# Optimization experiments

Hardware: AMD Instinct MI355X
Metric: run time of the kernel (lower is better)

The kernel has to match this reference:

```python
import jax, jax.numpy as jnp
import numpy as np

N = 20000      # nodes (human PPI network scale)
E = 640000     # edges (avg degree 32)
PE, GOS, PROT = 128, 128, 480
OM_DIMS = [3, 3, 24, 24]          # transcriptome, proteome, effectome, interactome
D = 384                           # latent_space_dimension = 128 * 3 (jk 'cat')
H = 128                           # hidden_channels per layer
NEG_SLOPE = 0.1


def setup_inputs() -> dict:
    key = jax.random.key(0)
    ks = jax.random.split(key, 64)
    rn = lambda k, shp, s=0.05: jax.random.normal(k, shp, jnp.float32) * s
    inp = {
        "x": jax.random.normal(ks[0], (N, PE + GOS + PROT), jnp.float32),
        "x_ft": jax.random.normal(ks[1], (N, sum(OM_DIMS)), jnp.float32),
        "edge_index": jax.random.randint(ks[2], (2, E), 0, N),
    }
    i = 3
    def lin(fin, fout, name):
        nonlocal i
        inp["W_" + name] = rn(ks[i], (fin, fout)); inp["b_" + name] = jnp.zeros((fout,), jnp.float32)
        i += 1
    lin(PE, D, "pe"); lin(GOS, D, "gos"); lin(PROT, D, "prot")
    for j, d in enumerate(OM_DIMS):
        lin(d, D, f"om{j}")
    dims = [D, H, H, H]
    for j in range(3):
        lin(dims[j], dims[j + 1], f"c{j}")   # feature-branch GCN convs
        lin(dims[j], dims[j + 1], f"o{j}")   # omics-branch GCN convs
    lin(2 * D, D, "lat")
    lin(D, H, "drug"); lin(D, H, "dis")
    lin(H, 2, "odrug"); lin(H, 2, "odis")
    return inp


def _gcn(x, W, b, src, dst, deg_inv):
    # GCNConv(improved=True): A_hat = A + 2I, sym norm D^-1/2 A_hat D^-1/2
    h = x @ W                                  # [N, F_out]
    coef = deg_inv[src] * deg_inv[dst]         # [E]
    agg = jax.ops.segment_sum(h[src] * coef[:, None], dst, num_segments=N)
    agg = agg + h * (2.0 * deg_inv * deg_inv)[:, None]   # self loops (weight 2)
    return agg + b


def reference(x, x_ft, edge_index,
              W_pe, b_pe, W_gos, b_gos, W_prot, b_prot,
              W_om0, b_om0, W_om1, b_om1, W_om2, b_om2, W_om3, b_om3,
              W_c0, b_c0, W_o0, b_o0, W_c1, b_c1, W_o1, b_o1, W_c2, b_c2, W_o2, b_o2,
              W_lat, b_lat, W_drug, b_drug, W_dis, b_dis,
              W_odrug, b_odrug, W_odis, b_odis):
    act = lambda t: jax.nn.leaky_relu(t, NEG_SLOPE)
    src, dst = edge_index[0], edge_index[1]
    deg = jax.ops.segment_sum(jnp.ones((E,), jnp.float32), dst, num_segments=N) + 2.0
    deg_inv = jax.lax.rsqrt(deg)

    # encoders (features branch): pe | gosemsim | prot_emb slices of x
    pe = x[:, :PE]; gos = x[:, PE:PE + GOS]; prot = x[:, PE + GOS:PE + GOS + PROT]
    h = act(pe @ W_pe + b_pe + gos @ W_gos + b_gos + prot @ W_prot + b_prot)

    # encoders (omics branch): 3|3|24|24 slices of x_ft
    offs = np.cumsum([0] + OM_DIMS)
    Wom = [W_om0, W_om1, W_om2, W_om3]; bom = [b_om0, b_om1, b_om2, b_om3]
    g = act(sum(x_ft[:, offs[j]:offs[j + 1]] @ Wom[j] + bom[j] for j in range(4)))

    Wc = [W_c0, W_c1, W_c2]; bc = [b_c0, b_c1, b_c2]
    Wo = [W_o0, W_o1, W_o2]; bo = [b_o0, b_o1, b_o2]
    hs, gs = [], []
    for j in range(3):
        h = act(_gcn(h, Wc[j], bc[j], src, dst, deg_inv)); hs.append(h)
        g = act(_gcn(g, Wo[j], bo[j], src, dst, deg_inv)); gs.append(g)
    jk = jnp.concatenate(hs, axis=-1)          # [N, 384]
    jk_om = jnp.concatenate(gs, axis=-1)       # [N, 384]

    z = act(jnp.concatenate([jk, jk_om], axis=-1) @ W_lat + b_lat)  # [N, 384]
    drug = act(z @ W_drug + b_drug) @ W_odrug + b_odrug             # [N, 2]
    dis = act(z @ W_dis + b_dis) @ W_odis + b_odis                  # [N, 2]
    return jnp.concatenate([drug, dis], axis=-1)                    # [N, 4]
```

## Files before the change

kernel.cpp:

```cpp
#include <hip/hip_runtime.h>
#include <cstdint>

#define NN 20000
#define NNP 20096
#define NE 640000
#define NEG_SLOPE 0.1f
#define NP4 4
#define PSZ 5000
#define CAP 48

typedef unsigned short ushort_t;
typedef __attribute__((ext_vector_type(8))) short short8;
typedef __attribute__((ext_vector_type(4))) float f32x4;

__device__ __forceinline__ unsigned short f2bf(float f) {
    union { float f; unsigned u; } v; v.f = f;
    unsigned r = v.u + 0x7fffu + ((v.u >> 16) & 1u);
    return (unsigned short)(r >> 16);
}
__device__ __forceinline__ float bflo(unsigned u) { return __uint_as_float(u << 16); }
__device__ __forceinline__ float bfhi(unsigned u) { return __uint_as_float(u & 0xffff0000u); }

__device__ __forceinline__ int swz(int r) { return (r ^ (r >> 2)) & 3; }

__device__ __forceinline__ void gld_lds16(const void* g, void* l) {
    __builtin_amdgcn_global_load_lds(
        (const __attribute__((address_space(1))) void*)g,
        (__attribute__((address_space(3))) void*)l,
        16, 0, 0);
}

#define O_CAT   0
#define O_OM    282624
#define O_C0    307200
#define O_O0    356352
#define O_C1    405504
#define O_O1    421888
#define O_C2    438272
#define O_O2    454656
#define O_LAT   471040
#define O_HEADS 765952
#define WT_TOTAL 864256

#define PACK_TOTAL (WT_TOTAL + 384 + 384 + 256)
#define CVT_T1 (NN * 736 / 4)
#define P1_FILLB (NE / 256)
#define P1_CVTB ((CVT_T1 + NN * 64 + 255) / 256)
#define P1_PKB  (PACK_TOTAL / 256)

__global__ __launch_bounds__(256) void phase1(
    const int* __restrict__ esrc, const int* __restrict__ edst,
    int* __restrict__ cnt4, unsigned* __restrict__ bkt,
    const float* __restrict__ x, const float* __restrict__ xft,
    ushort_t* __restrict__ xb, ushort_t* __restrict__ xftb,
    const float* __restrict__ Wpe, const float* __restrict__ Wgos, const float* __restrict__ Wprot,
    const float* __restrict__ bpe, const float* __restrict__ bgos, const float* __restrict__ bprot,
    const float* __restrict__ Wom0, const float* __restrict__ Wom1,
    const float* __restrict__ Wom2, const float* __restrict__ Wom3,
    const float* __restrict__ bom0, const float* __restrict__ bom1,
    const float* __restrict__ bom2, const float* __restrict__ bom3,
    const float* __restrict__ Wc0, const float* __restrict__ Wo0,
    const float* __restrict__ Wc1, const float* __restrict__ Wo1,
    const float* __restrict__ Wc2, const float* __restrict__ Wo2,
    const float* __restrict__ Wlat,
    const float* __restrict__ Wdrug, const float* __restrict__ Wdis,
    const float* __restrict__ bdrug, const float* __restrict__ bdis,
    ushort_t* __restrict__ Wt, float* __restrict__ bcat, float* __restrict__ bomc,
    float* __restrict__ bheads)
{
    int bx = blockIdx.x;
    if (bx < P1_FILLB) {
        int e = bx * 256 + threadIdx.x;
        int d = edst[e];
        int s = esrc[e];
        int p = (unsigned)s / (unsigned)PSZ;
        int pos = atomicAdd(&cnt4[d * NP4 + p], 1);
        if (pos < CAP)
            bkt[(d * NP4 + p) * CAP + pos] = (unsigned)s * 512u;
        return;
    }
    bx -= P1_FILLB;
    if (bx < P1_CVTB) {
        int i = bx * 256 + threadIdx.x;
        if (i < CVT_T1) {
            int base = i * 4;
            float4 v = *reinterpret_cast<const float4*>(&x[base]);
            unsigned long long p = (unsigned long long)f2bf(v.x)
                                 | ((unsigned long long)f2bf(v.y) << 16)
                                 | ((unsigned long long)f2bf(v.z) << 32)
                                 | ((unsigned long long)f2bf(v.w) << 48);
            *reinterpret_cast<unsigned long long*>(&xb[base]) = p;
            return;
        }
        i -= CVT_T1;
        if (i < NN * 64) {
            int r = i >> 6, c = i & 63;
            float v = (c < 54) ? xft[r * 54 + c] : 0.f;
            xftb[i] = f2bf(v);
        }
        return;
    }
    bx -= P1_CVTB;
    {
        int i = bx * 256 + threadIdx.x;
        if (i < 282624) {
            int m = i / 736, k = i % 736;
            float v = (k < 128) ? Wpe[k * 384 + m]
                    : (k < 256) ? Wgos[(k - 128) * 384 + m]
                                : Wprot[(k - 256) * 384 + m];
            Wt[O_CAT + i] = f2bf(v);
            return;
        }
        i -= 282624;
        if (i < 24576) {
            int m = i / 64, k = i % 64;
            float v = (k < 3)  ? Wom0[k * 384 + m]
                    : (k < 6)  ? Wom1[(k - 3) * 384 + m]
                    : (k < 30) ? Wom2[(k - 6) * 384 + m]
                    : (k < 54) ? Wom3[(k - 30) * 384 + m] : 0.f;
            Wt[O_OM + i] = f2bf(v);
            return;
        }
        i -= 24576;
        if (i < 49152) { int m = i / 384, k = i % 384; Wt[O_C0 + i] = f2bf(Wc0[k * 128 + m]); return; }
        i -= 49152;
        if (i < 49152) { int m = i / 384, k = i % 384; Wt[O_O0 + i] = f2bf(Wo0[k * 128 + m]); return; }
        i -= 49152;
        if (i < 16384) { int m = i / 128, k = i % 128; Wt[O_C1 + i] = f2bf(Wc1[k * 128 + m]); return; }
        i -= 16384;
        if (i < 16384) { int m = i / 128, k = i % 128; Wt[O_O1 + i] = f2bf(Wo1[k * 128 + m]); return; }
        i -= 16384;
        if (i < 16384) { int m = i / 128, k = i % 128; Wt[O_C2 + i] = f2bf(Wc2[k * 128 + m]); return; }
        i -= 16384;
        if (i < 16384) { int m = i / 128, k = i % 128; Wt[O_O2 + i] = f2bf(Wo2[k * 128 + m]); return; }
        i -= 16384;
        if (i < 294912) { int m = i / 768, k = i % 768; Wt[O_LAT + i] = f2bf(Wlat[k * 384 + m]); return; }
        i -= 294912;
        if (i < 98304) {
            int m = i / 384, k = i % 384;
            float v = (m < 128) ? Wdrug[k * 128 + m] : Wdis[k * 128 + (m - 128)];
            Wt[O_HEADS + i] = f2bf(v);
            return;
        }
        i -= 98304;
        if (i < 384) { bcat[i] = bpe[i] + bgos[i] + bprot[i]; return; }
        i -= 384;
        if (i < 384) { bomc[i] = bom0[i] + bom1[i] + bom2[i] + bom3[i]; return; }
        i -= 384;
        if (i < 256) { bheads[i] = (i < 128) ? bdrug[i] : bdis[i - 128]; return; }
    }
}

template<int BN>
__device__ __forceinline__ void gemm_core(
    ushort_t* As, ushort_t* Bs,
    const ushort_t* __restrict__ A, int lda,
    const ushort_t* __restrict__ Wt, int K, int row0, int col0,
    f32x4 (&acc)[4][(BN == 128) ? 4 : 2])
{
    constexpr int BK = 32;
    constexpr int NI = (BN == 128) ? 4 : 2;

    const int t = threadIdx.x;
    const int w = t >> 6, lane = t & 63;
    const int wr = w >> 1, wc = w & 1;
    const int m16 = lane & 15, quad = lane >> 4;
    const int sr = lane >> 2;
    const int pgrp = lane & 3;

#pragma unroll
    for (int mi = 0; mi < 4; mi++)
#pragma unroll
        for (int ni = 0; ni < NI; ni++) acc[mi][ni] = (f32x4)0.f;

    for (int k0 = 0; k0 < K; k0 += BK) {
#pragma unroll
        for (int p = 0; p < 2; p++) {
            int c = p * 4 + w;
            int r = c * 16 + sr;
            int q = pgrp ^ swz(r);
            gld_lds16(&A[(size_t)(row0 + r) * lda + k0 + q * 8], &As[c * 512]);
        }
#pragma unroll
        for (int p = 0; p < BN / 64; p++) {
            int c = p * 4 + w;
            int r = c * 16 + sr;
            int q = pgrp ^ swz(r);
            gld_lds16(&Wt[(size_t)(col0 + r) * K + k0 + q * 8], &Bs[c * 512]);
        }
        __syncthreads();

        short8 af[4], bfr[NI];
#pragma unroll
        for (int mi = 0; mi < 4; mi++) {
            int r = wr * 64 + mi * 16 + m16;
            int p = quad ^ swz(r);
            af[mi] = *reinterpret_cast<const short8*>(&As[r * 32 + p * 8]);
        }
#pragma unroll
        for (int ni = 0; ni < NI; ni++) {
            int n = wc * (NI * 16) + ni * 16 + m16;
            int p = quad ^ swz(n);
            bfr[ni] = *reinterpret_cast<const short8*>(&Bs[n * 32 + p * 8]);
        }
#pragma unroll
        for (int mi = 0; mi < 4; mi++)
#pragma unroll
            for (int ni = 0; ni < NI; ni++)
                acc[mi][ni] = __builtin_amdgcn_mfma_f32_16x16x32_bf16(af[mi], bfr[ni], acc[mi][ni], 0, 0, 0);
        __syncthreads();
    }
}

template<int BN, bool BIASACT, bool OUT_BF16>
__device__ __forceinline__ void gemm_store(
    const f32x4 (&acc)[4][(BN == 128) ? 4 : 2],
    const float* __restrict__ bias,
    float* __restrict__ Cf, ushort_t* __restrict__ Cb, int ldc,
    int nrows, int row0, int col0)
{
    constexpr int NI = (BN == 128) ? 4 : 2;
    const int t = threadIdx.x;
    const int w = t >> 6, lane = t & 63;
    const int wr = w >> 1, wc = w & 1;
    const int m16 = lane & 15, quad = lane >> 4;
#pragma unroll
    for (int mi = 0; mi < 4; mi++) {
#pragma unroll
        for (int reg = 0; reg < 4; reg++) {
            int grow = row0 + wr * 64 + mi * 16 + quad * 4 + reg;
            if (grow >= nrows) continue;
#pragma unroll
            for (int ni = 0; ni < NI; ni++) {
                int gcol = col0 + wc * (NI * 16) + ni * 16 + m16;
                float v = acc[mi][ni][reg];
                if constexpr (BIASACT) {
                    v += bias[gcol];
                    v = (v > 0.f) ? v : NEG_SLOPE * v;
                }
                if constexpr (OUT_BF16) Cb[(size_t)grow * ldc + gcol] = f2bf(v);
                else                    Cf[(size_t)grow * ldc + gcol] = v;
            }
        }
    }
}

template<int BN, bool BIASACT, bool OUT_BF16>
__global__ __launch_bounds__(256) void mfma_gemm(
    const ushort_t* __restrict__ A, int lda,
    const ushort_t* __restrict__ Wt,
    const float* __restrict__ bias,
    float* __restrict__ Cf, ushort_t* __restrict__ Cb, int ldc,
    int nrows, int K)
{
    __shared__ ushort_t As[128 * 32];
    __shared__ ushort_t Bs[BN * 32];
    f32x4 acc[4][(BN == 128) ? 4 : 2];
    gemm_core<BN>(As, Bs, A, lda, Wt, K, blockIdx.y * 128, blockIdx.x * BN, acc);
    gemm_store<BN, BIASACT, OUT_BF16>(acc, bias, Cf, Cb, ldc, nrows,
                                      blockIdx.y * 128, blockIdx.x * BN);
}

#define MD_DGB 79
#define MD_MLPB (3 * 157 * 2)
__global__ __launch_bounds__(256) void mlp_deginv(
    const int* __restrict__ cnt4, float* __restrict__ deg_inv,
    const ushort_t* __restrict__ xb, const ushort_t* __restrict__ xftb,
    const ushort_t* __restrict__ Wt,
    const float* __restrict__ bcat, const float* __restrict__ bomc,
    ushort_t* __restrict__ h0b, ushort_t* __restrict__ g0b)
{
    __shared__ ushort_t As[128 * 32];
    __shared__ ushort_t Bs[128 * 32];
    int bx = blockIdx.x;
    if (bx < MD_DGB) {
        int i = bx * 256 + threadIdx.x;
        if (i < NN) {
            int4 c = *reinterpret_cast<const int4*>(&cnt4[i * NP4]);
            deg_inv[i] = rsqrtf((float)(c.x + c.y + c.z + c.w) + 2.0f);
        }
        return;
    }
    bx -= MD_DGB;
    int z = bx / 471, r = bx % 471;
    int by = r / 3, b3 = r % 3;
    f32x4 acc[4][4];
    const int row0 = by * 128, col0 = b3 * 128;
    if (z == 0) {
        gemm_core<128>(As, Bs, xb, 736, Wt + O_CAT, 736, row0, col0, acc);
        gemm_store<128, true, true>(acc, bcat, nullptr, h0b, 384, NN, row0, col0);
    } else {
        gemm_core<128>(As, Bs, xftb, 64, Wt + O_OM, 64, row0, col0, acc);
        gemm_store<128, true, true>(acc, bomc, nullptr, g0b, 384, NN, row0, col0);
    }
}

__global__ __launch_bounds__(256) void mfma_gemm_dual(
    const ushort_t* __restrict__ A0, const ushort_t* __restrict__ A1, int lda,
    const ushort_t* __restrict__ W0, const ushort_t* __restrict__ W1,
    ushort_t* __restrict__ tmpI,
    int nrows, int K)
{
    __shared__ ushort_t As[128 * 32];
    __shared__ ushort_t Bs[64 * 32];
    const ushort_t* A  = blockIdx.z ? A1 : A0;
    const ushort_t* Wt = blockIdx.z ? W1 : W0;
    ushort_t*       Cb = tmpI + blockIdx.z * 128;
    f32x4 acc[4][2];
    gemm_core<64>(As, Bs, A, lda, Wt, K, blockIdx.y * 128, blockIdx.x * 64, acc);
    gemm_store<64, false, true>(acc, nullptr, nullptr, Cb, 256, nrows,
                                blockIdx.y * 128, blockIdx.x * 64);
}

__global__ __launch_bounds__(256) void mfma_gemm_heads(
    const ushort_t* __restrict__ zb, const ushort_t* __restrict__ Wt,
    const float* __restrict__ bheads,
    const float* __restrict__ Wod, const float* __restrict__ bod,
    const float* __restrict__ Wos, const float* __restrict__ bos,
    float* __restrict__ out)
{
    __shared__ ushort_t As[128 * 32];
    __shared__ ushort_t Bs[128 * 32];
    f32x4 acc[4][4];
    const int row0 = blockIdx.y * 128, col0 = blockIdx.x * 128;
    gemm_core<128>(As, Bs, zb, 384, Wt + O_HEADS, 384, row0, col0, acc);

    const float* __restrict__ Wh = col0 ? Wos : Wod;
    const float* __restrict__ bh = col0 ? bos : bod;
    const int t = threadIdx.x;
    const int w = t >> 6, lane = t & 63;
    const int wr = w >> 1, wc = w & 1;
    const int m16 = lane & 15, quad = lane >> 4;

    float w0[4], w1[4];
#pragma unroll
    for (int ni = 0; ni < 4; ni++) {
        int k = wc * 64 + ni * 16 + m16;
        w0[ni] = Wh[k * 2 + 0];
        w1[ni] = Wh[k * 2 + 1];
    }
    float p0[16], p1[16];
#pragma unroll
    for (int mi = 0; mi < 4; mi++) {
#pragma unroll
        for (int reg = 0; reg < 4; reg++) {
            float s0 = 0.f, s1 = 0.f;
#pragma unroll
            for (int ni = 0; ni < 4; ni++) {
                int gcol = col0 + wc * 64 + ni * 16 + m16;
                float v = acc[mi][ni][reg] + bheads[gcol];
                v = (v > 0.f) ? v : NEG_SLOPE * v;
                s0 = fmaf(v, w0[ni], s0);
                s1 = fmaf(v, w1[ni], s1);
            }
            p0[mi * 4 + reg] = s0;
            p1[mi * 4 + reg] = s1;
        }
    }
#pragma unroll
    for (int m = 1; m <= 8; m <<= 1) {
#pragma unroll
        for (int idx = 0; idx < 16; idx++) {
            p0[idx] += __shfl_xor(p0[idx], m);
            p1[idx] += __shfl_xor(p1[idx], m);
        }
    }
    float* red = reinterpret_cast<float*>(As);
    if (m16 == 0) {
#pragma unroll
        for (int mi = 0; mi < 4; mi++)
#pragma unroll
            for (int reg = 0; reg < 4; reg++) {
                int row = mi * 16 + quad * 4 + reg;
                int base = (((wr * 2 + wc) * 64) + row) * 2;
                red[base + 0] = p0[mi * 4 + reg];
                red[base + 1] = p1[mi * 4 + reg];
            }
    }
    __syncthreads();
    if (t < 128) {
        int wr2 = t >> 6, row = t & 63;
        int grow = row0 + wr2 * 64 + row;
        if (grow < NN) {
            int b0 = ((wr2 * 2 + 0) * 64 + row) * 2;
            int b1 = ((wr2 * 2 + 1) * 64 + row) * 2;
            float o0 = red[b0 + 0] + red[b1 + 0] + bh[0];
            float o1 = red[b0 + 1] + red[b1 + 1] + bh[1];
            out[(size_t)grow * 4 + (col0 ? 2 : 0) + 0] = o0;
            out[(size_t)grow * 4 + (col0 ? 2 : 0) + 1] = o1;
        }
    }
}

__global__ __launch_bounds__(256) void aggregate_fused(
    const ushort_t* __restrict__ tabI,
    const float* __restrict__ bc, const float* __restrict__ bo,
    const int* __restrict__ cnt4, const unsigned* __restrict__ bkt,
    const float* __restrict__ deg_inv,
    ushort_t* __restrict__ outb, int hcol, int gcol)
{
    const int w = threadIdx.x >> 6, lane = threadIdx.x & 63;
    const int i = blockIdx.x * 4 + w;
    const int el = lane >> 5;
    const int fq = lane & 31;
    const int chain = fq >> 4;
    const unsigned lbyte = (unsigned)(fq * 16);
    const char* __restrict__ tb = (const char*)tabI;

    const float di = deg_inv[i];
    const uint4 pv = *reinterpret_cast<const uint4*>(tb + ((unsigned)i * 512u + lbyte));
    const int4 cc = *reinterpret_cast<const int4*>(&cnt4[i * NP4]);
    const int cn[4] = {cc.x, cc.y, cc.z, cc.w};
    const unsigned* __restrict__ bb = &bkt[(size_t)i * NP4 * CAP];

    float acc[8];
#pragma unroll
    for (int q = 0; q < 8; q++) acc[q] = 0.f;

#define FMA8(P, C) \
    acc[0] = fmaf(bflo(P.x), C, acc[0]); acc[1] = fmaf(bfhi(P.x), C, acc[1]); \
    acc[2] = fmaf(bflo(P.y), C, acc[2]); acc[3] = fmaf(bfhi(P.y), C, acc[3]); \
    acc[4] = fmaf(bflo(P.z), C, acc[4]); acc[5] = fmaf(bfhi(P.z), C, acc[5]); \
    acc[6] = fmaf(bflo(P.w), C, acc[6]); acc[7] = fmaf(bfhi(P.w), C, acc[7])

#pragma unroll
    for (int p = 0; p < NP4; p++) {
        const unsigned* __restrict__ bp = bb + p * CAP;
        const int n = cn[p];
        int j = el;
        for (; j + 6 < n; j += 8) {
            unsigned s0 = bp[j], s1 = bp[j + 2], s2 = bp[j + 4], s3 = bp[j + 6];
            uint4 p0 = *reinterpret_cast<const uint4*>(tb + (s0 + lbyte));
            uint4 p1 = *reinterpret_cast<const uint4*>(tb + (s1 + lbyte));
            uint4 p2 = *reinterpret_cast<const uint4*>(tb + (s2 + lbyte));
            uint4 p3 = *reinterpret_cast<const uint4*>(tb + (s3 + lbyte));
            float c0 = deg_inv[s0 >> 9] * di;
            float c1 = deg_inv[s1 >> 9] * di;
            float c2 = deg_inv[s2 >> 9] * di;
            float c3 = deg_inv[s3 >> 9] * di;
            FMA8(p0, c0); FMA8(p1, c1); FMA8(p2, c2); FMA8(p3, c3);
        }
        if (j < n) {
            int l = n - 1;
            unsigned s0 = bp[j];
            unsigned s1 = bp[(j + 2 < n) ? j + 2 : l];
            unsigned s2 = bp[(j + 4 < n) ? j + 4 : l];
            unsigned s3 = bp[(j + 6 < n) ? j + 6 : l];
            uint4 p0 = *reinterpret_cast<const uint4*>(tb + (s0 + lbyte));
            uint4 p1 = *reinterpret_cast<const uint4*>(tb + (s1 + lbyte));
            uint4 p2 = *reinterpret_cast<const uint4*>(tb + (s2 + lbyte));
            uint4 p3 = *reinterpret_cast<const uint4*>(tb + (s3 + lbyte));
            float c0 = deg_inv[s0 >> 9] * di;
            float c1 = (j + 2 < n) ? deg_inv[s1 >> 9] * di : 0.f;
            float c2 = (j + 4 < n) ? deg_inv[s2 >> 9] * di : 0.f;
            float c3 = (j + 6 < n) ? deg_inv[s3 >> 9] * di : 0.f;
            FMA8(p0, c0); FMA8(p1, c1); FMA8(p2, c2); FMA8(p3, c3);
        }
    }
#undef FMA8

#pragma unroll
    for (int q = 0; q < 8; q++) acc[q] += __shfl_xor(acc[q], 32);

    if (el == 0) {
        const float* __restrict__ bias = chain ? bo : bc;
        const int coloff = (fq & 15) * 8;
        const float c = 2.f * di * di;
        float sv[8] = {bflo(pv.x), bfhi(pv.x), bflo(pv.y), bfhi(pv.y),
                       bflo(pv.z), bfhi(pv.z), bflo(pv.w), bfhi(pv.w)};
        uint4 o;
        unsigned* op = &o.x;
#pragma unroll
        for (int q = 0; q < 8; q += 2) {
            float v0 = fmaf(sv[q],     c, acc[q])     + bias[coloff + q];
            float v1 = fmaf(sv[q + 1], c, acc[q + 1]) + bias[coloff + q + 1];
            v0 = (v0 > 0.f) ? v0 : NEG_SLOPE * v0;
            v1 = (v1 > 0.f) ? v1 : NEG_SLOPE * v1;
            op[q >> 1] = (unsigned)f2bf(v0) | ((unsigned)f2bf(v1) << 16);
        }
        const int col = (chain ? gcol : hcol) + coloff;
        *reinterpret_cast<uint4*>(&outb[(size_t)i * 768 + col]) = o;
    }
}

extern "C" void kernel_launch(void* const* d_in, const int* in_sizes, int n_in,
                              void* d_out, int out_size, void* d_ws, size_t ws_size,
                              hipStream_t stream)
{
    const float* x      = (const float*)d_in[0];
    const float* x_ft   = (const float*)d_in[1];
    const int*   eidx   = (const int*)d_in[2];
    const float* W_pe   = (const float*)d_in[3];
    const float* b_pe   = (const float*)d_in[4];
    const float* W_gos  = (const float*)d_in[5];
    const float* b_gos  = (const float*)d_in[6];
    const float* W_prot = (const float*)d_in[7];
    const float* b_prot = (const float*)d_in[8];
    const float* W_om0  = (const float*)d_in[9];
    const float* b_om0  = (const float*)d_in[10];
    const float* W_om1  = (const float*)d_in[11];
    const float* b_om1  = (const float*)d_in[12];
    const float* W_om2  = (const float*)d_in[13];
    const float* b_om2  = (const float*)d_in[14];
    const float* W_om3  = (const float*)d_in[15];
    const float* b_om3  = (const float*)d_in[16];
    const float* W_c[3] = {(const float*)d_in[17], (const float*)d_in[21], (const float*)d_in[25]};
    const float* b_c[3] = {(const float*)d_in[18], (const float*)d_in[22], (const float*)d_in[26]};
    const float* W_o[3] = {(const float*)d_in[19], (const float*)d_in[23], (const float*)d_in[27]};
    const float* b_o[3] = {(const float*)d_in[20], (const float*)d_in[24], (const float*)d_in[28]};
    const float* W_lat  = (const float*)d_in[29];
    const float* b_lat  = (const float*)d_in[30];
    const float* W_drug = (const float*)d_in[31];
    const float* b_drug = (const float*)d_in[32];
    const float* W_dis  = (const float*)d_in[33];
    const float* b_dis  = (const float*)d_in[34];
    const float* W_odrug= (const float*)d_in[35];
    const float* b_odrug= (const float*)d_in[36];
    const float* W_odis = (const float*)d_in[37];
    const float* b_odis = (const float*)d_in[38];
    float* out = (float*)d_out;

    const int* e_src = eidx;
    const int* e_dst = eidx + NE;

    char* p = (char*)d_ws;
    auto alloc = [&](size_t bytes) -> void* {
        void* r = (void*)p;
        p += (bytes + 255) & ~(size_t)255;
        return r;
    };
    ushort_t* Wt    = (ushort_t*)alloc((size_t)WT_TOTAL * 2);
    float* bcat     = (float*)alloc(384 * 4);
    float* bomc     = (float*)alloc(384 * 4);
    float* bheads   = (float*)alloc(256 * 4);
    float* deg_inv  = (float*)alloc((size_t)NN * 4);
    int*   cnt4     = (int*)alloc((size_t)NN * NP4 * 4);
    unsigned* bkt   = (unsigned*)alloc((size_t)NN * NP4 * CAP * 4);
    ushort_t* xb    = (ushort_t*)alloc((size_t)NNP * 736 * 2);
    ushort_t* xftb  = (ushort_t*)alloc((size_t)NNP * 64 * 2);
    ushort_t* h0b   = (ushort_t*)alloc((size_t)NNP * 384 * 2);
    ushort_t* g0b   = (ushort_t*)alloc((size_t)NNP * 384 * 2);
    ushort_t* jkb   = (ushort_t*)alloc((size_t)NNP * 768 * 2);
    ushort_t* zb    = (ushort_t*)alloc((size_t)NNP * 384 * 2);
    ushort_t* tmpI  = (ushort_t*)alloc((size_t)NNP * 256 * 2);
    (void)ws_size; (void)in_sizes; (void)n_in; (void)out_size;

    hipMemsetAsync(cnt4, 0, (size_t)NN * NP4 * 4, stream);
    phase1<<<dim3(P1_FILLB + P1_CVTB + P1_PKB), dim3(256), 0, stream>>>(
        e_src, e_dst, cnt4, bkt,
        x, x_ft, xb, xftb,
        W_pe, W_gos, W_prot, b_pe, b_gos, b_prot,
        W_om0, W_om1, W_om2, W_om3, b_om0, b_om1, b_om2, b_om3,
        W_c[0], W_o[0], W_c[1], W_o[1], W_c[2], W_o[2],
        W_lat, W_drug, W_dis, b_drug, b_dis, Wt, bcat, bomc, bheads);

    mlp_deginv<<<dim3(MD_DGB + MD_MLPB), dim3(256), 0, stream>>>(
        cnt4, deg_inv, xb, xftb, Wt, bcat, bomc, h0b, g0b);

    mfma_gemm_dual<<<dim3(2, 157, 2), dim3(256), 0, stream>>>(
        h0b, g0b, 384, Wt + O_C0, Wt + O_O0, tmpI, NN, 384);
    aggregate_fused<<<dim3(NN / 4), dim3(256), 0, stream>>>(
        tmpI, b_c[0], b_o[0], cnt4, bkt, deg_inv, jkb, 0, 384);

    mfma_gemm_dual<<<dim3(2, 157, 2), dim3(256), 0, stream>>>(
        jkb + 0, jkb + 384, 768, Wt + O_C1, Wt + O_O1, tmpI, NN, 128);
    aggregate_fused<<<dim3(NN / 4), dim3(256), 0, stream>>>(
        tmpI, b_c[1], b_o[1], cnt4, bkt, deg_inv, jkb, 128, 512);

    mfma_gemm_dual<<<dim3(2, 157, 2), dim3(256), 0, stream>>>(
        jkb + 128, jkb + 512, 768, Wt + O_C2, Wt + O_O2, tmpI, NN, 128);
    aggregate_fused<<<dim3(NN / 4), dim3(256), 0, stream>>>(
        tmpI, b_c[2], b_o[2], cnt4, bkt, deg_inv, jkb, 256, 640);

    mfma_gemm<128, true, true><<<dim3(3, 157), dim3(256), 0, stream>>>(
        jkb, 768, Wt + O_LAT, b_lat, nullptr, zb, 384, NN, 768);

    mfma_gemm_heads<<<dim3(2, 157), dim3(256), 0, stream>>>(
        zb, Wt, bheads, W_odrug, b_odrug, W_odis, b_odis, out);
}
```

Measured before the change: 429.5 us.

## Merge post-phase1 kernels into one cooperative persistent kernel with grid syncs

Replaces the eight separate launches (MLP/deg_inv, three dual GEMM + aggregate pairs, latent GEMM, heads GEMM) with a single cooperative persistent kernel. The blocks loop over work tiles and separate the stages with grid.sync(). The aim is to remove launch overhead and the gaps between kernels. In exchange, every stage is capped at the co-resident block count, shared memory is sized for the largest stage, and grid-wide barriers may cost more than kernel boundaries.

```diff
diff --git a/kernel.cpp b/kernel.cpp
--- a/kernel.cpp
+++ b/kernel.cpp
@@ -1,5 +1,8 @@
 #include <hip/hip_runtime.h>
+#include <hip/hip_cooperative_groups.h>
 #include <cstdint>
+
+namespace cg = cooperative_groups;
 
 #define NN 20000
 #define NNP 20096
@@ -245,162 +248,15 @@
     }
 }
 
-template<int BN, bool BIASACT, bool OUT_BF16>
-__global__ __launch_bounds__(256) void mfma_gemm(
-    const ushort_t* __restrict__ A, int lda,
-    const ushort_t* __restrict__ Wt,
-    const float* __restrict__ bias,
-    float* __restrict__ Cf, ushort_t* __restrict__ Cb, int ldc,
-    int nrows, int K)
-{
-    __shared__ ushort_t As[128 * 32];
-    __shared__ ushort_t Bs[BN * 32];
-    f32x4 acc[4][(BN == 128) ? 4 : 2];
-    gemm_core<BN>(As, Bs, A, lda, Wt, K, blockIdx.y * 128, blockIdx.x * BN, acc);
-    gemm_store<BN, BIASACT, OUT_BF16>(acc, bias, Cf, Cb, ldc, nrows,
-                                      blockIdx.y * 128, blockIdx.x * BN);
-}
-
-#define MD_DGB 79
-#define MD_MLPB (3 * 157 * 2)
-__global__ __launch_bounds__(256) void mlp_deginv(
-    const int* __restrict__ cnt4, float* __restrict__ deg_inv,
-    const ushort_t* __restrict__ xb, const ushort_t* __restrict__ xftb,
-    const ushort_t* __restrict__ Wt,
-    const float* __restrict__ bcat, const float* __restrict__ bomc,
-    ushort_t* __restrict__ h0b, ushort_t* __restrict__ g0b)
-{
-    __shared__ ushort_t As[128 * 32];
-    __shared__ ushort_t Bs[128 * 32];
-    int bx = blockIdx.x;
-    if (bx < MD_DGB) {
-        int i = bx * 256 + threadIdx.x;
-        if (i < NN) {
-            int4 c = *reinterpret_cast<const int4*>(&cnt4[i * NP4]);
-            deg_inv[i] = rsqrtf((float)(c.x + c.y + c.z + c.w) + 2.0f);
-        }
-        return;
-    }
-    bx -= MD_DGB;
-    int z = bx / 471, r = bx % 471;
-    int by = r / 3, b3 = r % 3;
-    f32x4 acc[4][4];
-    const int row0 = by * 128, col0 = b3 * 128;
-    if (z == 0) {
-        gemm_core<128>(As, Bs, xb, 736, Wt + O_CAT, 736, row0, col0, acc);
-        gemm_store<128, true, true>(acc, bcat, nullptr, h0b, 384, NN, row0, col0);
-    } else {
-        gemm_core<128>(As, Bs, xftb, 64, Wt + O_OM, 64, row0, col0, acc);
-        gemm_store<128, true, true>(acc, bomc, nullptr, g0b, 384, NN, row0, col0);
-    }
-}
-
-__global__ __launch_bounds__(256) void mfma_gemm_dual(
-    const ushort_t* __restrict__ A0, const ushort_t* __restrict__ A1, int lda,
-    const ushort_t* __restrict__ W0, const ushort_t* __restrict__ W1,
-    ushort_t* __restrict__ tmpI,
-    int nrows, int K)
-{
-    __shared__ ushort_t As[128 * 32];
-    __shared__ ushort_t Bs[64 * 32];
-    const ushort_t* A  = blockIdx.z ? A1 : A0;
-    const ushort_t* Wt = blockIdx.z ? W1 : W0;
-    ushort_t*       Cb = tmpI + blockIdx.z * 128;
-    f32x4 acc[4][2];
-    gemm_core<64>(As, Bs, A, lda, Wt, K, blockIdx.y * 128, blockIdx.x * 64, acc);
-    gemm_store<64, false, true>(acc, nullptr, nullptr, Cb, 256, nrows,
-                                blockIdx.y * 128, blockIdx.x * 64);
-}
-
-__global__ __launch_bounds__(256) void mfma_gemm_heads(
-    const ushort_t* __restrict__ zb, const ushort_t* __restrict__ Wt,
-    const float* __restrict__ bheads,
-    const float* __restrict__ Wod, const float* __restrict__ bod,
-    const float* __restrict__ Wos, const float* __restrict__ bos,
-    float* __restrict__ out)
-{
-    __shared__ ushort_t As[128 * 32];
-    __shared__ ushort_t Bs[128 * 32];
-    f32x4 acc[4][4];
-    const int row0 = blockIdx.y * 128, col0 = blockIdx.x * 128;
-    gemm_core<128>(As, Bs, zb, 384, Wt + O_HEADS, 384, row0, col0, acc);
-
-    const float* __restrict__ Wh = col0 ? Wos : Wod;
-    const float* __restrict__ bh = col0 ? bos : bod;
-    const int t = threadIdx.x;
-    const int w = t >> 6, lane = t & 63;
-    const int wr = w >> 1, wc = w & 1;
-    const int m16 = lane & 15, quad = lane >> 4;
-
-    float w0[4], w1[4];
-#pragma unroll
-    for (int ni = 0; ni < 4; ni++) {
-        int k = wc * 64 + ni * 16 + m16;
-        w0[ni] = Wh[k * 2 + 0];
-        w1[ni] = Wh[k * 2 + 1];
-    }
-    float p0[16], p1[16];
-#pragma unroll
-    for (int mi = 0; mi < 4; mi++) {
-#pragma unroll
-        for (int reg = 0; reg < 4; reg++) {
-            float s0 = 0.f, s1 = 0.f;
-#pragma unroll
-            for (int ni = 0; ni < 4; ni++) {
-                int gcol = col0 + wc * 64 + ni * 16 + m16;
-                float v = acc[mi][ni][reg] + bheads[gcol];
-                v = (v > 0.f) ? v : NEG_SLOPE * v;
-                s0 = fmaf(v, w0[ni], s0);
-                s1 = fmaf(v, w1[ni], s1);
-            }
-            p0[mi * 4 + reg] = s0;
-            p1[mi * 4 + reg] = s1;
-        }
-    }
-#pragma unroll
-    for (int m = 1; m <= 8; m <<= 1) {
-#pragma unroll
-        for (int idx = 0; idx < 16; idx++) {
-            p0[idx] += __shfl_xor(p0[idx], m);
-            p1[idx] += __shfl_xor(p1[idx], m);
-        }
-    }
-    float* red = reinterpret_cast<float*>(As);
-    if (m16 == 0) {
-#pragma unroll
-        for (int mi = 0; mi < 4; mi++)
-#pragma unroll
-            for (int reg = 0; reg < 4; reg++) {
-                int row = mi * 16 + quad * 4 + reg;
-                int base = (((wr * 2 + wc) * 64) + row) * 2;
-                red[base + 0] = p0[mi * 4 + reg];
-                red[base + 1] = p1[mi * 4 + reg];
-            }
-    }
-    __syncthreads();
-    if (t < 128) {
-        int wr2 = t >> 6, row = t & 63;
-        int grow = row0 + wr2 * 64 + row;
-        if (grow < NN) {
-            int b0 = ((wr2 * 2 + 0) * 64 + row) * 2;
-            int b1 = ((wr2 * 2 + 1) * 64 + row) * 2;
-            float o0 = red[b0 + 0] + red[b1 + 0] + bh[0];
-            float o1 = red[b0 + 1] + red[b1 + 1] + bh[1];
-            out[(size_t)grow * 4 + (col0 ? 2 : 0) + 0] = o0;
-            out[(size_t)grow * 4 + (col0 ? 2 : 0) + 1] = o1;
-        }
-    }
-}
-
-__global__ __launch_bounds__(256) void aggregate_fused(
+__device__ __forceinline__ void aggregate_body(
     const ushort_t* __restrict__ tabI,
     const float* __restrict__ bc, const float* __restrict__ bo,
     const int* __restrict__ cnt4, const unsigned* __restrict__ bkt,
     const float* __restrict__ deg_inv,
-    ushort_t* __restrict__ outb, int hcol, int gcol)
+    ushort_t* __restrict__ outb, int hcol, int gcol, int blk)
 {
     const int w = threadIdx.x >> 6, lane = threadIdx.x & 63;
-    const int i = blockIdx.x * 4 + w;
+    const int i = blk * 4 + w;
     const int el = lane >> 5;
     const int fq = lane & 31;
     const int chain = fq >> 4;
@@ -480,6 +336,171 @@
         }
         const int col = (chain ? gcol : hcol) + coloff;
         *reinterpret_cast<uint4*>(&outb[(size_t)i * 768 + col]) = o;
+    }
+}
+
+struct MegaP {
+    const int* cnt4; float* deg_inv;
+    const ushort_t* xb; const ushort_t* xftb; const ushort_t* Wt;
+    const float* bcat; const float* bomc;
+    ushort_t* h0b; ushort_t* g0b;
+    ushort_t* jkb; ushort_t* zb; ushort_t* tmpI;
+    const unsigned* bkt;
+    const float* bc0; const float* bo0;
+    const float* bc1; const float* bo1;
+    const float* bc2; const float* bo2;
+    const float* b_lat; const float* bheads;
+    const float* Wod; const float* bod;
+    const float* Wos; const float* bos;
+    float* out;
+};
+
+#define MD_DGB 79
+#define MD_MLPB (3 * 157 * 2)
+
+__global__ __launch_bounds__(256, 4) void mega(MegaP P)
+{
+    cg::grid_group grid = cg::this_grid();
+    __shared__ ushort_t As[128 * 32];
+    __shared__ ushort_t Bs[128 * 32];
+    const int NB = (int)gridDim.x;
+
+    for (int it = blockIdx.x; it < MD_DGB + MD_MLPB; it += NB) {
+        if (it < MD_DGB) {
+            int i = it * 256 + threadIdx.x;
+            if (i < NN) {
+                int4 c = *reinterpret_cast<const int4*>(&P.cnt4[i * NP4]);
+                P.deg_inv[i] = rsqrtf((float)(c.x + c.y + c.z + c.w) + 2.0f);
+            }
+            continue;
+        }
+        int b = it - MD_DGB;
+        int z = b / 471, r = b % 471;
+        int by = r / 3, b3 = r % 3;
+        f32x4 acc[4][4];
+        const int row0 = by * 128, col0 = b3 * 128;
+        if (z == 0) {
+            gemm_core<128>(As, Bs, P.xb, 736, P.Wt + O_CAT, 736, row0, col0, acc);
+            gemm_store<128, true, true>(acc, P.bcat, nullptr, P.h0b, 384, NN, row0, col0);
+        } else {
+            gemm_core<128>(As, Bs, P.xftb, 64, P.Wt + O_OM, 64, row0, col0, acc);
+            gemm_store<128, true, true>(acc, P.bomc, nullptr, P.g0b, 384, NN, row0, col0);
+        }
+    }
+    grid.sync();
+
+    const ushort_t* dA0[3] = {P.h0b, P.jkb + 0,   P.jkb + 128};
+    const ushort_t* dA1[3] = {P.g0b, P.jkb + 384, P.jkb + 512};
+    const int dlda[3] = {384, 768, 768};
+    const int dK[3]   = {384, 128, 128};
+    const int dW0[3]  = {O_C0, O_C1, O_C2};
+    const int dW1[3]  = {O_O0, O_O1, O_O2};
+    const float* abc[3] = {P.bc0, P.bc1, P.bc2};
+    const float* abo[3] = {P.bo0, P.bo1, P.bo2};
+    const int hcolA[3] = {0, 128, 256};
+    const int gcolA[3] = {384, 512, 640};
+
+#pragma unroll 1
+    for (int L = 0; L < 3; L++) {
+        for (int it = blockIdx.x; it < 2 * 157 * 2; it += NB) {
+            int z = it & 1, rr = it >> 1;
+            int bxx = rr & 1, by = rr >> 1;
+            const ushort_t* A  = z ? dA1[L] : dA0[L];
+            const ushort_t* W  = P.Wt + (z ? dW1[L] : dW0[L]);
+            ushort_t*       Cb = P.tmpI + z * 128;
+            f32x4 acc[4][2];
+            gemm_core<64>(As, Bs, A, dlda[L], W, dK[L], by * 128, bxx * 64, acc);
+            gemm_store<64, false, true>(acc, nullptr, nullptr, Cb, 256, NN,
+                                        by * 128, bxx * 64);
+        }
+        grid.sync();
+        for (int it = blockIdx.x; it < NN / 4; it += NB) {
+            aggregate_body(P.tmpI, abc[L], abo[L], P.cnt4, P.bkt, P.deg_inv,
+                           P.jkb, hcolA[L], gcolA[L], it);
+        }
+        grid.sync();
+    }
+
+    for (int it = blockIdx.x; it < 3 * 157; it += NB) {
+        int b3 = it % 3, by = it / 3;
+        f32x4 acc[4][4];
+        gemm_core<128>(As, Bs, P.jkb, 768, P.Wt + O_LAT, 768, by * 128, b3 * 128, acc);
+        gemm_store<128, true, true>(acc, P.b_lat, nullptr, P.zb, 384, NN, by * 128, b3 * 128);
+    }
+    grid.sync();
+
+    for (int it = blockIdx.x; it < 2 * 157; it += NB) {
+        int cx = it & 1, by = it >> 1;
+        const int row0 = by * 128, col0 = cx * 128;
+        f32x4 acc[4][4];
+        gemm_core<128>(As, Bs, P.zb, 384, P.Wt + O_HEADS, 384, row0, col0, acc);
+
+        const float* __restrict__ Wh = col0 ? P.Wos : P.Wod;
+        const float* __restrict__ bh = col0 ? P.bos : P.bod;
+        const int t = threadIdx.x;
+        const int w = t >> 6, lane = t & 63;
+        const int wr = w >> 1, wc = w & 1;
+        const int m16 = lane & 15, quad = lane >> 4;
+
+        float w0[4], w1[4];
+#pragma unroll
+        for (int ni = 0; ni < 4; ni++) {
+            int k = wc * 64 + ni * 16 + m16;
+            w0[ni] = Wh[k * 2 + 0];
+            w1[ni] = Wh[k * 2 + 1];
+        }
+        float p0[16], p1[16];
+#pragma unroll
+        for (int mi = 0; mi < 4; mi++) {
+#pragma unroll
+            for (int reg = 0; reg < 4; reg++) {
+                float s0 = 0.f, s1 = 0.f;
+#pragma unroll
+                for (int ni = 0; ni < 4; ni++) {
+                    int gcol = col0 + wc * 64 + ni * 16 + m16;
+                    float v = acc[mi][ni][reg] + P.bheads[gcol];
+                    v = (v > 0.f) ? v : NEG_SLOPE * v;
+                    s0 = fmaf(v, w0[ni], s0);
+                    s1 = fmaf(v, w1[ni], s1);
+                }
+                p0[mi * 4 + reg] = s0;
+                p1[mi * 4 + reg] = s1;
+            }
+        }
+#pragma unroll
+        for (int m = 1; m <= 8; m <<= 1) {
+#pragma unroll
+            for (int idx = 0; idx < 16; idx++) {
+                p0[idx] += __shfl_xor(p0[idx], m);
+                p1[idx] += __shfl_xor(p1[idx], m);
+            }
+        }
+        float* red = reinterpret_cast<float*>(As);
+        if (m16 == 0) {
+#pragma unroll
+            for (int mi = 0; mi < 4; mi++)
+#pragma unroll
+                for (int reg = 0; reg < 4; reg++) {
+                    int row = mi * 16 + quad * 4 + reg;
+                    int base = (((wr * 2 + wc) * 64) + row) * 2;
+                    red[base + 0] = p0[mi * 4 + reg];
+                    red[base + 1] = p1[mi * 4 + reg];
+                }
+        }
+        __syncthreads();
+        if (t < 128) {
+            int wr2 = t >> 6, row = t & 63;
+            int grow = row0 + wr2 * 64 + row;
+            if (grow < NN) {
+                int b0 = ((wr2 * 2 + 0) * 64 + row) * 2;
+                int b1 = ((wr2 * 2 + 1) * 64 + row) * 2;
+                float o0 = red[b0 + 0] + red[b1 + 0] + bh[0];
+                float o1 = red[b0 + 1] + red[b1 + 1] + bh[1];
+                P.out[(size_t)grow * 4 + (col0 ? 2 : 0) + 0] = o0;
+                P.out[(size_t)grow * 4 + (col0 ? 2 : 0) + 1] = o1;
+            }
+        }
+        __syncthreads();
     }
 }
 
@@ -554,27 +575,28 @@
         W_c[0], W_o[0], W_c[1], W_o[1], W_c[2], W_o[2],
         W_lat, W_drug, W_dis, b_drug, b_dis, Wt, bcat, bomc, bheads);
 
-    mlp_deginv<<<dim3(MD_DGB + MD_MLPB), dim3(256), 0, stream>>>(
-        cnt4, deg_inv, xb, xftb, Wt, bcat, bomc, h0b, g0b);
-
-    mfma_gemm_dual<<<dim3(2, 157, 2), dim3(256), 0, stream>>>(
-        h0b, g0b, 384, Wt + O_C0, Wt + O_O0, tmpI, NN, 384);
-    aggregate_fused<<<dim3(NN / 4), dim3(256), 0, stream>>>(
-        tmpI, b_c[0], b_o[0], cnt4, bkt, deg_inv, jkb, 0, 384);
-
-    mfma_gemm_dual<<<dim3(2, 157, 2), dim3(256), 0, stream>>>(
-        jkb + 0, jkb + 384, 768, Wt + O_C1, Wt + O_O1, tmpI, NN, 128);
-    aggregate_fused<<<dim3(NN / 4), dim3(256), 0, stream>>>(
-        tmpI, b_c[1], b_o[1], cnt4, bkt, deg_inv, jkb, 128, 512);
-
-    mfma_gemm_dual<<<dim3(2, 157, 2), dim3(256), 0, stream>>>(
-        jkb + 128, jkb + 512, 768, Wt + O_C2, Wt + O_O2, tmpI, NN, 128);
-    aggregate_fused<<<dim3(NN / 4), dim3(256), 0, stream>>>(
-        tmpI, b_c[2], b_o[2], cnt4, bkt, deg_inv, jkb, 256, 640);
-
-    mfma_gemm<128, true, true><<<dim3(3, 157), dim3(256), 0, stream>>>(
-        jkb, 768, Wt + O_LAT, b_lat, nullptr, zb, 384, NN, 768);
-
-    mfma_gemm_heads<<<dim3(2, 157), dim3(256), 0, stream>>>(
-        zb, Wt, bheads, W_odrug, b_odrug, W_odis, b_odis, out);
-}
+    MegaP ma;
+    ma.cnt4 = cnt4; ma.deg_inv = deg_inv;
+    ma.xb = xb; ma.xftb = xftb; ma.Wt = Wt;
+    ma.bcat = bcat; ma.bomc = bomc;
+    ma.h0b = h0b; ma.g0b = g0b;
+    ma.jkb = jkb; ma.zb = zb; ma.tmpI = tmpI;
+    ma.bkt = bkt;
+    ma.bc0 = b_c[0]; ma.bo0 = b_o[0];
+    ma.bc1 = b_c[1]; ma.bo1 = b_o[1];
+    ma.bc2 = b_c[2]; ma.bo2 = b_o[2];
+    ma.b_lat = b_lat; ma.bheads = bheads;
+    ma.Wod = W_odrug; ma.bod = b_odrug;
+    ma.Wos = W_odis;  ma.bos = b_odis;
+    ma.out = out;
+
+    int nbPerCU = 0;
+    if (hipOccupancyMaxActiveBlocksPerMultiprocessor(&nbPerCU, mega, 256, 0)
+            != hipSuccess || nbPerCU < 1)
+        nbPerCU = 2;
+    int nblk = nbPerCU * 256;
+    if (nblk > 1280) nblk = 1280;
+
+    void* kargs[] = { (void*)&ma };
+    hipLaunchCooperativeKernel(mega, dim3(nblk), dim3(256), kargs, 0, stream);
+}
```

New measurement: 1.080 ms. 2.51x slower.
